# Optimization experiments

Hardware: AMD Instinct MI355X
Metric: run time of the kernel (lower is better)

## Reference

```python
import jax, jax.numpy as jnp
import numpy as np

UNITS = 1024
IN_DIM = 1024
BATCH = 64
SEQ = 512


def setup_inputs() -> dict:
    key = jax.random.key(0)
    k_x, k_wf, k_wb = jax.random.split(key, 3)
    x = jax.random.normal(k_x, (BATCH, SEQ, IN_DIM), dtype=jnp.float32)
    # keras 'random_normal' initializer -> stddev 0.05
    W_fwd = jax.random.normal(k_wf, (IN_DIM + UNITS, 4 * UNITS), dtype=jnp.float32) * 0.05
    b_fwd = jnp.zeros((4 * UNITS,), dtype=jnp.float32)
    W_bwd = jax.random.normal(k_wb, (IN_DIM + UNITS, 4 * UNITS), dtype=jnp.float32) * 0.05
    b_bwd = jnp.zeros((4 * UNITS,), dtype=jnp.float32)
    return {"x": x, "W_fwd": W_fwd, "b_fwd": b_fwd, "W_bwd": W_bwd, "b_bwd": b_bwd}


def _lstm_scan(x_tbd, W, b, units, reverse):
    # x_tbd: [T, B, D] time-major
    B = x_tbd.shape[1]
    h0 = jnp.zeros((B, units), dtype=x_tbd.dtype)
    c0 = jnp.zeros((B, units), dtype=x_tbd.dtype)

    def step(carry, x_t):
        h, c = carry
        z = jnp.concatenate([x_t, h], axis=-1) @ W + b  # [B, 4U]
        zi, zf, zo, zg = jnp.split(z, 4, axis=-1)
        c_new = jax.nn.sigmoid(zf) * c + jax.nn.sigmoid(zi) * jnp.tanh(zg)
        h_new = jax.nn.sigmoid(zo) * jnp.tanh(c_new)
        return (h_new, c_new), h_new

    _, hs = jax.lax.scan(step, (h0, c0), x_tbd, reverse=reverse)
    return hs  # [T, B, U], aligned with input time order


def reference(x, W_fwd, b_fwd, W_bwd, b_bwd):
    x_tbd = jnp.transpose(x, (1, 0, 2))  # [T, B, D]
    h_fwd = _lstm_scan(x_tbd, W_fwd, b_fwd, UNITS, reverse=False)
    h_bwd = _lstm_scan(x_tbd, W_bwd, b_bwd, UNITS, reverse=True)
    h = jnp.concatenate([h_fwd, h_bwd], axis=-1)  # [T, B, 2U]
    return jnp.transpose(h, (1, 0, 2))  # [B, T, 2U]
```

## Files before the change

kernel.cpp:

```cpp
#include <hip/hip_runtime.h>
#include <stdint.h>

#define B_ 64
#define T_ 512
#define D_ 1024
#define U_ 1024
#define G4_ 4096
#define M_ (B_ * T_)
#define ZLD 65

typedef unsigned short u16;
typedef float f32x4 __attribute__((ext_vector_type(4)));
typedef _Float16 f16x8 __attribute__((ext_vector_type(8)));
typedef unsigned short u16x4 __attribute__((ext_vector_type(4)));

__device__ __forceinline__ u16 f2h(float f) {
  union { _Float16 h; u16 u; } v; v.h = (_Float16)f; return v.u;
}
__device__ __forceinline__ float h2f(uint32_t u) {
  union { _Float16 h; u16 u; } v; v.u = (u16)u; return (float)v.h;
}
__device__ __forceinline__ float sigm(float x) { return 1.f / (1.f + __expf(-x)); }
__device__ __forceinline__ float tanhf_(float x) {
  x = fminf(12.f, fmaxf(-12.f, x));
  float e = __expf(2.f * x);
  return (e - 1.f) / (e + 1.f);
}

__device__ __forceinline__ void glds16(const void* g, void* l) {
  __builtin_amdgcn_global_load_lds(
      (const __attribute__((address_space(1))) uint32_t*)g,
      (__attribute__((address_space(3))) uint32_t*)l, 16, 0, 0);
}

template <int R>
__device__ __forceinline__ void stage_tile(const char* gbase, long gs, char* lds, int tid) {
  const int lane = tid & 63, wid = tid >> 6;
#pragma unroll
  for (int j = wid; j < R / 8; j += 4) {
    const int row = j * 8 + (lane >> 3);
    const int lg = ((lane & 7) * 16) ^ ((row & 7) << 4);
    glds16(gbase + (long)row * gs + lg, lds + j * 1024);
  }
}

__device__ __forceinline__ f16x8 read_frag(const char* lds, int row, int kbyte) {
  const int ph = row * 128 + (kbyte ^ ((row & 7) << 4));
  return *(const f16x8*)(lds + ph);
}

#define MFMA_(a, b, c) __builtin_amdgcn_mfma_f32_16x16x32_f16(a, b, c, 0, 0, 0)


__global__ __launch_bounds__(256) void cast_x_kernel(const float* __restrict__ x,
                                                     u16* __restrict__ xb) {
  const long n = (long)M_ * D_ / 4;
  for (long i = (long)blockIdx.x * blockDim.x + threadIdx.x; i < n;
       i += (long)gridDim.x * blockDim.x) {
    f32x4 v = ((const f32x4*)x)[i];
    u16x4 r;
#pragma unroll
    for (int j = 0; j < 4; ++j) r[j] = f2h(v[j]);
    ((u16x4*)xb)[i] = r;
  }
}

__global__ __launch_bounds__(256) void pack_wx_kernel(const float* __restrict__ Wf,
                                                      const float* __restrict__ Wb,
                                                      u16* __restrict__ wxT) {
  const int idx = blockIdx.x * 256 + threadIdx.x;
  const int p = idx & 4095;
  const int kc = (idx >> 12) & 63;
  const int d = (idx >> 18) & 1;
  const float* W = d ? Wb : Wf;
  const int orig = ((p >> 4) & 3) * 1024 + ((p >> 6) << 4) + (p & 15);
  u16* dst = wxT + ((long)d * G4_ + p) * 1024 + kc * 16;
  const float* src = W + (long)(kc * 16) * G4_ + orig;
#pragma unroll
  for (int j = 0; j < 16; ++j) dst[j] = f2h(src[(long)j * G4_]);
}

__global__ __launch_bounds__(256) void pack_whfl_kernel(const float* __restrict__ Wf,
                                                        const float* __restrict__ Wb,
                                                        u16* __restrict__ whfl) {
  const int idx = blockIdx.x * 256 + threadIdx.x;
  const int l = idx & 63;
  const int f = (idx >> 6) & 15;
  const int cc = (idx >> 10) & 7;
  const int ub = (idx >> 13) & 63;
  const int d = (idx >> 19) & 1;
  const float* W = d ? Wb : Wf;
  const int ni = f >> 2, kkl = f & 3;
  const int ocol = ni * 1024 + ub * 16 + (l & 15);
  const int krow = 1024 + cc * 128 + kkl * 32 + (l >> 4) * 8;
  u16* dst = whfl + ((((long)(d * 64 + ub) * 8 + cc) * 16 + f) << 9) + l * 8;
  const float* src = W + (long)krow * G4_ + ocol;
#pragma unroll
  for (int j = 0; j < 8; ++j) dst[j] = f2h(src[(long)j * G4_]);
}

__global__ __launch_bounds__(256) void gemm_xproj2(const u16* __restrict__ xbf,
                                                   const u16* __restrict__ wT,
                                                   const float* __restrict__ bF,
                                                   const float* __restrict__ bB,
                                                   u16* __restrict__ xp2) {
  __shared__ __align__(16) char smem[64 * 1024];
  const int tid = threadIdx.x, lane = tid & 63, wid = tid >> 6;
  const int wr = wid >> 1, wc = wid & 1;
  const int tm = blockIdx.x * 128, tn = blockIdx.y * 128, d = blockIdx.z;
  const char* Ag = (const char*)xbf + (long)tm * 2048;
  const char* Bg = (const char*)wT + ((long)d * G4_ + tn) * 2048;

  f32x4 acc[4][4];
#pragma unroll
  for (int mi = 0; mi < 4; ++mi)
#pragma unroll
    for (int ni = 0; ni < 4; ++ni)
#pragma unroll
      for (int v = 0; v < 4; ++v) acc[mi][ni][v] = 0.f;

  stage_tile<128>(Ag, 2048, smem, tid);
  stage_tile<128>(Bg, 2048, smem + 32768, tid);
  __syncthreads();
  const int rA = lane & 15, kb = (lane >> 4) * 16;

  for (int cc = 0; cc < 16; ++cc) {
    const int cur = cc & 1;
    char* Ac = smem + cur * 16384;
    char* Bc = smem + 32768 + cur * 16384;
    if (cc + 1 < 16) {
      stage_tile<128>(Ag + (cc + 1) * 128, 2048, smem + (cur ^ 1) * 16384, tid);
      stage_tile<128>(Bg + (cc + 1) * 128, 2048, smem + 32768 + (cur ^ 1) * 16384, tid);
    }
    f16x8 aF[4][2], bFr[4][2];
#pragma unroll
    for (int mi = 0; mi < 4; ++mi)
#pragma unroll
      for (int ks = 0; ks < 2; ++ks)
        aF[mi][ks] = read_frag(Ac, wr * 64 + mi * 16 + rA, kb + ks * 64);
#pragma unroll
    for (int ni = 0; ni < 4; ++ni)
#pragma unroll
      for (int ks = 0; ks < 2; ++ks)
        bFr[ni][ks] = read_frag(Bc, wc * 64 + ni * 16 + rA, kb + ks * 64);
#pragma unroll
    for (int mi = 0; mi < 4; ++mi)
#pragma unroll
      for (int ni = 0; ni < 4; ++ni)
#pragma unroll
        for (int ks = 0; ks < 2; ++ks)
          acc[mi][ni] = MFMA_(aF[mi][ks], bFr[ni][ks], acc[mi][ni]);
    __syncthreads();
  }

  const float* bias = d ? bB : bF;
#pragma unroll
  for (int ni = 0; ni < 4; ++ni) {
    const int p = tn + wc * 64 + ni * 16 + rA;
    const int orig = ((p >> 4) & 3) * 1024 + ((p >> 6) << 4) + (p & 15);
    const float bv = bias[orig];
    const int ub2 = p >> 6, pl = p & 63;
#pragma unroll
    for (int mi = 0; mi < 4; ++mi) {
      const int m0 = tm + wr * 64 + mi * 16 + (lane >> 4) * 4;
#pragma unroll
      for (int v = 0; v < 4; ++v) {
        const int m = m0 + v, b = m >> 9, t = m & 511;
        const int bh = b >> 5, br = b & 31;
        xp2[(((((long)d * T_ + t) * 64 + ub2) * 2 + bh) * 32 + br) * 64 + pl] =
            f2h(acc[mi][ni][v] + bv);
      }
    }
  }
}


__device__ __forceinline__ void stage_hA(const char* g, char* lds, int tid) {
  const int lane = tid & 63, wid = tid >> 6;
#pragma unroll
  for (int q = 0; q < 16; ++q) {
    const int idx = wid + q * 4;
    const int row = idx * 8 + (lane >> 3);
    const int off = ((lane & 7) * 16) ^ (((row >> 4) & 7) << 4);
    glds16(g + (long)row * 128 + off, lds + idx * 1024);
  }
}

__device__ __forceinline__ void stage_Bc(const char* wfl, int cc, char* slot, int tid) {
  const int lane = tid & 63, wid = tid >> 6;
#pragma unroll
  for (int q = 0; q < 4; ++q) {
    const int f = wid * 4 + q;
    glds16(wfl + (long)cc * 16384 + f * 1024 + lane * 16, slot + f * 1024);
  }
}

template <int CC>
__device__ __forceinline__ void kstep(char* smem, const char* wfl, int tid,
                                      int wr, int wc, int rA, int kq,
                                      f32x4 (&acc)[2]) {
  constexpr int REM = 7 - CC;
  constexpr int N = 4 * (REM < 3 ? REM : 3);
  asm volatile("s_waitcnt vmcnt(%0)" :: "i"(N) : "memory");
  __builtin_amdgcn_s_barrier();
  asm volatile("" ::: "memory");
  const char* A = smem;
  const char* Bslot = smem + 65536 + (CC & 3) * 16384;
  const int lane16 = (tid & 63) << 4;
  f16x8 aF[4], bF[2][4];
  const int br = wr * 16 + rA;
#pragma unroll
  for (int ks = 0; ks < 4; ++ks) {
    const int kbyte = CC * 256 + ks * 64 + kq * 16;
    aF[ks] = *(const f16x8*)(A + br * 2048 + (kbyte ^ ((br & 7) << 4)));
  }
#pragma unroll
  for (int ni = 0; ni < 2; ++ni)
#pragma unroll
    for (int ks = 0; ks < 4; ++ks)
      bF[ni][ks] = *(const f16x8*)(Bslot + ((wc * 2 + ni) * 4 + ks) * 1024 + lane16);
#pragma unroll
  for (int ni = 0; ni < 2; ++ni)
#pragma unroll
    for (int ks = 0; ks < 4; ++ks)
      acc[ni] = MFMA_(aF[ks], bF[ni][ks], acc[ni]);
  asm volatile("s_waitcnt lgkmcnt(0)" ::: "memory");
  __builtin_amdgcn_sched_barrier(0);
  __builtin_amdgcn_s_barrier();
  asm volatile("" ::: "memory");
  if (CC + 4 < 8)
    stage_Bc(wfl, CC + 4, smem + 65536 + ((CC + 4) & 3) * 16384, tid);
}

__global__ __launch_bounds__(256) void lstm_step8(
    const u16* __restrict__ whfl, const u16* __restrict__ xp2,
    const u16* __restrict__ h_read, u16* __restrict__ h_write,
    float* __restrict__ cst, float* __restrict__ out, int s) {
  __shared__ __align__(16) char smem[131072 + ZLD * 32 * 4];
  float* zbuf = (float*)(smem + 131072);
  const int tid = threadIdx.x, lane = tid & 63, wid = tid >> 6;
  const int wr = wid >> 1, wc = wid & 1;
  const int g = blockIdx.x, ub = g >> 1, d = g & 1, bh = blockIdx.y;
  const int t = d ? (T_ - 1 - s) : s;
  const char* hA = (const char*)h_read + ((long)d * B_ + bh * 32) * 2048;
  const char* wfl = (const char*)whfl + ((long)(d * 64 + ub) << 17);
  const char* xg = (const char*)xp2 + ((((long)d * T_ + t) * 64 + ub) * 2 + bh) * 4096;
  const int rA = lane & 15, kq = lane >> 4;

  const int bl_g = tid >> 3, ui_g = (tid & 7) * 2;
  const int u_g = ub * 16 + ui_g;
  const int bglob = bh * 32 + bl_g;

  uint32_t xr[4];
  const char* xt = xg + (bl_g * 64 + ui_g) * 2;
#define XL(gg)                                                          \
  asm volatile("global_load_dword %0, %1, off offset:%2"               \
               : "=v"(xr[gg]) : "v"(xt), "n"(gg * 32) : "memory")
  XL(0); XL(1); XL(2); XL(3);
#undef XL
  stage_hA(hA, smem, tid);
#pragma unroll
  for (int c0 = 0; c0 < 4; ++c0)
    stage_Bc(wfl, c0, smem + 65536 + c0 * 16384, tid);

  const float2 creg = *(const float2*)(cst + ((long)d * B_ + bglob) * 1024 + u_g);

  f32x4 acc[2];
#pragma unroll
  for (int ni = 0; ni < 2; ++ni)
#pragma unroll
    for (int v = 0; v < 4; ++v) acc[ni][v] = 0.f;

  kstep<0>(smem, wfl, tid, wr, wc, rA, kq, acc);
  kstep<1>(smem, wfl, tid, wr, wc, rA, kq, acc);
  kstep<2>(smem, wfl, tid, wr, wc, rA, kq, acc);
  kstep<3>(smem, wfl, tid, wr, wc, rA, kq, acc);
  kstep<4>(smem, wfl, tid, wr, wc, rA, kq, acc);
  kstep<5>(smem, wfl, tid, wr, wc, rA, kq, acc);
  kstep<6>(smem, wfl, tid, wr, wc, rA, kq, acc);
  kstep<7>(smem, wfl, tid, wr, wc, rA, kq, acc);

#pragma unroll
  for (int ni = 0; ni < 2; ++ni)
#pragma unroll
    for (int v = 0; v < 4; ++v) {
      const int row = wr * 16 + kq * 4 + v;
      const int col = (wc * 2 + ni) * 16 + rA;
      zbuf[row * ZLD + col] = acc[ni][v];
    }
  __syncthreads();

  {
    const float* zb = zbuf + bl_g * ZLD + ui_g;
    const float zi0 = zb[0]  + h2f(xr[0] & 0xffff);
    const float zi1 = zb[1]  + h2f(xr[0] >> 16);
    const float zf0 = zb[16] + h2f(xr[1] & 0xffff);
    const float zf1 = zb[17] + h2f(xr[1] >> 16);
    const float zo0 = zb[32] + h2f(xr[2] & 0xffff);
    const float zo1 = zb[33] + h2f(xr[2] >> 16);
    const float zg0 = zb[48] + h2f(xr[3] & 0xffff);
    const float zg1 = zb[49] + h2f(xr[3] >> 16);
    const float cn0 = sigm(zf0) * creg.x + sigm(zi0) * tanhf_(zg0);
    const float cn1 = sigm(zf1) * creg.y + sigm(zi1) * tanhf_(zg1);
    const float hn0 = sigm(zo0) * tanhf_(cn0);
    const float hn1 = sigm(zo1) * tanhf_(cn1);

    float2 cw; cw.x = cn0; cw.y = cn1;
    *(float2*)(cst + ((long)d * B_ + bglob) * 1024 + u_g) = cw;
    const uint32_t hv = (uint32_t)f2h(hn0) | ((uint32_t)f2h(hn1) << 16);
    *(uint32_t*)(h_write + ((long)d * B_ + bglob) * 1024 + u_g) = hv;
    float2 o2; o2.x = hn0; o2.y = hn1;
    *(float2*)(out + ((long)bglob * T_ + t) * 2048 + d * 1024 + u_g) = o2;
  }
}


extern "C" void kernel_launch(void* const* d_in, const int* in_sizes, int n_in,
                              void* d_out, int out_size, void* d_ws, size_t ws_size,
                              hipStream_t stream) {
  const float* x = (const float*)d_in[0];
  const float* Wf = (const float*)d_in[1];
  const float* bfp = (const float*)d_in[2];
  const float* Wb = (const float*)d_in[3];
  const float* bbp = (const float*)d_in[4];
  float* out = (float*)d_out;
  char* ws = (char*)d_ws;

  size_t off = 0;
  auto alloc = [&](size_t bytes) {
    char* p = ws + off;
    off = (off + bytes + 255) & ~(size_t)255;
    return p;
  };
  u16* xbf = (u16*)alloc((size_t)M_ * D_ * 2);
  u16* wxT = (u16*)alloc((size_t)2 * G4_ * 1024 * 2);
  u16* whfl = (u16*)alloc((size_t)2 * 64 * 128 * 1024);
  u16* hst = (u16*)alloc((size_t)2 * 2 * B_ * U_ * 2);
  float* cst = (float*)alloc((size_t)2 * B_ * U_ * 4);
  u16* xproj = (u16*)alloc((size_t)2 * B_ * T_ * G4_ * 2);

  hipMemsetAsync(hst, 0, (size_t)2 * 2 * B_ * U_ * 2, stream);
  hipMemsetAsync(cst, 0, (size_t)2 * B_ * U_ * 4, stream);

  cast_x_kernel<<<2048, 256, 0, stream>>>(x, xbf);
  pack_wx_kernel<<<2048, 256, 0, stream>>>(Wf, Wb, wxT);
  pack_whfl_kernel<<<4096, 256, 0, stream>>>(Wf, Wb, whfl);

  dim3 gg(M_ / 128, G4_ / 128, 2);
  gemm_xproj2<<<gg, 256, 0, stream>>>(xbf, wxT, bfp, bbp, xproj);

  for (int s = 0; s < T_; ++s) {
    const u16* hr = hst + (size_t)(s & 1) * 2 * B_ * U_;
    u16* hw = hst + (size_t)((s + 1) & 1) * 2 * B_ * U_;
    lstm_step8<<<dim3(128, 2), 256, 0, stream>>>(whfl, xproj, hr, hw, cst, out, s);
  }
}
```

Before: 3.999 ms.

## Load h fragments directly to registers and split K across warps

The per-timestep recurrent kernel stops staging h through LDS. Each lane loads its A fragments straight from global memory into registers, and all of the W_h tile is staged into LDS in one pass instead of a 4-slot ring. The work is re-split so pairs of warps each take half of K, with the partial sums reduced through the LDS z buffer. This removes the eight barrier-separated k-steps and their pipelined waits, which is where the serial per-step latency was spent. The cost is one long wait for all loads before any MFMA starts, plus higher register use for 16 fragment vectors.

```diff
diff --git a/kernel.cpp b/kernel.cpp
--- a/kernel.cpp
+++ b/kernel.cpp
@@ -50,6 +50,7 @@
 }
 
 #define MFMA_(a, b, c) __builtin_amdgcn_mfma_f32_16x16x32_f16(a, b, c, 0, 0, 0)
+#define BAR_LGKM() asm volatile("s_waitcnt lgkmcnt(0)\n\ts_barrier" ::: "memory")
 
 
 __global__ __launch_bounds__(256) void cast_x_kernel(const float* __restrict__ x,
@@ -174,78 +175,19 @@
   }
 }
 
-
-__device__ __forceinline__ void stage_hA(const char* g, char* lds, int tid) {
-  const int lane = tid & 63, wid = tid >> 6;
-#pragma unroll
-  for (int q = 0; q < 16; ++q) {
-    const int idx = wid + q * 4;
-    const int row = idx * 8 + (lane >> 3);
-    const int off = ((lane & 7) * 16) ^ (((row >> 4) & 7) << 4);
-    glds16(g + (long)row * 128 + off, lds + idx * 1024);
-  }
-}
-
-__device__ __forceinline__ void stage_Bc(const char* wfl, int cc, char* slot, int tid) {
-  const int lane = tid & 63, wid = tid >> 6;
-#pragma unroll
-  for (int q = 0; q < 4; ++q) {
-    const int f = wid * 4 + q;
-    glds16(wfl + (long)cc * 16384 + f * 1024 + lane * 16, slot + f * 1024);
-  }
-}
-
-template <int CC>
-__device__ __forceinline__ void kstep(char* smem, const char* wfl, int tid,
-                                      int wr, int wc, int rA, int kq,
-                                      f32x4 (&acc)[2]) {
-  constexpr int REM = 7 - CC;
-  constexpr int N = 4 * (REM < 3 ? REM : 3);
-  asm volatile("s_waitcnt vmcnt(%0)" :: "i"(N) : "memory");
-  __builtin_amdgcn_s_barrier();
-  asm volatile("" ::: "memory");
-  const char* A = smem;
-  const char* Bslot = smem + 65536 + (CC & 3) * 16384;
-  const int lane16 = (tid & 63) << 4;
-  f16x8 aF[4], bF[2][4];
-  const int br = wr * 16 + rA;
-#pragma unroll
-  for (int ks = 0; ks < 4; ++ks) {
-    const int kbyte = CC * 256 + ks * 64 + kq * 16;
-    aF[ks] = *(const f16x8*)(A + br * 2048 + (kbyte ^ ((br & 7) << 4)));
-  }
-#pragma unroll
-  for (int ni = 0; ni < 2; ++ni)
-#pragma unroll
-    for (int ks = 0; ks < 4; ++ks)
-      bF[ni][ks] = *(const f16x8*)(Bslot + ((wc * 2 + ni) * 4 + ks) * 1024 + lane16);
-#pragma unroll
-  for (int ni = 0; ni < 2; ++ni)
-#pragma unroll
-    for (int ks = 0; ks < 4; ++ks)
-      acc[ni] = MFMA_(aF[ks], bF[ni][ks], acc[ni]);
-  asm volatile("s_waitcnt lgkmcnt(0)" ::: "memory");
-  __builtin_amdgcn_sched_barrier(0);
-  __builtin_amdgcn_s_barrier();
-  asm volatile("" ::: "memory");
-  if (CC + 4 < 8)
-    stage_Bc(wfl, CC + 4, smem + 65536 + ((CC + 4) & 3) * 16384, tid);
-}
-
-__global__ __launch_bounds__(256) void lstm_step8(
+__global__ __launch_bounds__(256) void lstm_step9(
     const u16* __restrict__ whfl, const u16* __restrict__ xp2,
     const u16* __restrict__ h_read, u16* __restrict__ h_write,
     float* __restrict__ cst, float* __restrict__ out, int s) {
   __shared__ __align__(16) char smem[131072 + ZLD * 32 * 4];
   float* zbuf = (float*)(smem + 131072);
   const int tid = threadIdx.x, lane = tid & 63, wid = tid >> 6;
-  const int wr = wid >> 1, wc = wid & 1;
+  const int wm = wid & 1, kh = wid >> 1;
   const int g = blockIdx.x, ub = g >> 1, d = g & 1, bh = blockIdx.y;
   const int t = d ? (T_ - 1 - s) : s;
-  const char* hA = (const char*)h_read + ((long)d * B_ + bh * 32) * 2048;
+  const int rA = lane & 15, kq = lane >> 4;
   const char* wfl = (const char*)whfl + ((long)(d * 64 + ub) << 17);
   const char* xg = (const char*)xp2 + ((((long)d * T_ + t) * 64 + ub) * 2 + bh) * 4096;
-  const int rA = lane & 15, kq = lane >> 4;
 
   const int bl_g = tid >> 3, ui_g = (tid & 7) * 2;
   const int u_g = ub * 16 + ui_g;
@@ -258,37 +200,62 @@
                : "=v"(xr[gg]) : "v"(xt), "n"(gg * 32) : "memory")
   XL(0); XL(1); XL(2); XL(3);
 #undef XL
-  stage_hA(hA, smem, tid);
-#pragma unroll
-  for (int c0 = 0; c0 < 4; ++c0)
-    stage_Bc(wfl, c0, smem + 65536 + c0 * 16384, tid);
-
+  const char* ah_base =
+      (const char*)h_read +
+      (((long)d * B_ + bh * 32 + wm * 16 + rA) * 1024 + kh * 512 + kq * 8) * 2;
+  f16x8 ah[16];
+#define AH(i)                                                           \
+  asm volatile("global_load_dwordx4 %0, %1, off offset:%2"             \
+               : "=v"(ah[i]) : "v"(ah_base), "n"(i * 64) : "memory")
+  AH(0); AH(1); AH(2); AH(3); AH(4); AH(5); AH(6); AH(7);
+  AH(8); AH(9); AH(10); AH(11); AH(12); AH(13); AH(14); AH(15);
+#undef AH
+#pragma unroll
+  for (int q = 0; q < 32; ++q) {
+    const int f = wid * 32 + q;
+    glds16(wfl + (long)f * 1024 + lane * 16, smem + f * 1024);
+  }
   const float2 creg = *(const float2*)(cst + ((long)d * B_ + bglob) * 1024 + u_g);
 
-  f32x4 acc[2];
-#pragma unroll
-  for (int ni = 0; ni < 2; ++ni)
+  asm volatile("s_waitcnt vmcnt(0)" ::: "memory");
+  __builtin_amdgcn_sched_barrier(0);
+  __builtin_amdgcn_s_barrier();
+  asm volatile("" ::: "memory");
+
+  f32x4 acc[4];
+#pragma unroll
+  for (int ni = 0; ni < 4; ++ni)
 #pragma unroll
     for (int v = 0; v < 4; ++v) acc[ni][v] = 0.f;
-
-  kstep<0>(smem, wfl, tid, wr, wc, rA, kq, acc);
-  kstep<1>(smem, wfl, tid, wr, wc, rA, kq, acc);
-  kstep<2>(smem, wfl, tid, wr, wc, rA, kq, acc);
-  kstep<3>(smem, wfl, tid, wr, wc, rA, kq, acc);
-  kstep<4>(smem, wfl, tid, wr, wc, rA, kq, acc);
-  kstep<5>(smem, wfl, tid, wr, wc, rA, kq, acc);
-  kstep<6>(smem, wfl, tid, wr, wc, rA, kq, acc);
-  kstep<7>(smem, wfl, tid, wr, wc, rA, kq, acc);
-
-#pragma unroll
-  for (int ni = 0; ni < 2; ++ni)
-#pragma unroll
-    for (int v = 0; v < 4; ++v) {
-      const int row = wr * 16 + kq * 4 + v;
-      const int col = (wc * 2 + ni) * 16 + rA;
-      zbuf[row * ZLD + col] = acc[ni][v];
+  const char* bb = smem + (kh << 16) + (lane << 4);
+#pragma unroll
+  for (int kk = 0; kk < 16; ++kk) {
+#pragma unroll
+    for (int ni = 0; ni < 4; ++ni) {
+      const f16x8 bF =
+          *(const f16x8*)(bb + (((kk >> 2) * 16 + ni * 4 + (kk & 3)) << 10));
+      acc[ni] = MFMA_(ah[kk], bF, acc[ni]);
     }
-  __syncthreads();
+  }
+
+  if (kh == 1) {
+#pragma unroll
+    for (int ni = 0; ni < 4; ++ni)
+#pragma unroll
+      for (int v = 0; v < 4; ++v)
+        zbuf[(wm * 16 + kq * 4 + v) * ZLD + ni * 16 + rA] = acc[ni][v];
+  }
+  BAR_LGKM();
+  if (kh == 0) {
+#pragma unroll
+    for (int ni = 0; ni < 4; ++ni)
+#pragma unroll
+      for (int v = 0; v < 4; ++v) {
+        const int ix = (wm * 16 + kq * 4 + v) * ZLD + ni * 16 + rA;
+        zbuf[ix] += acc[ni][v];
+      }
+  }
+  BAR_LGKM();
 
   {
     const float* zb = zbuf + bl_g * ZLD + ui_g;
@@ -352,6 +319,6 @@
   for (int s = 0; s < T_; ++s) {
     const u16* hr = hst + (size_t)(s & 1) * 2 * B_ * U_;
     u16* hw = hst + (size_t)((s + 1) & 1) * 2 * B_ * U_;
-    lstm_step8<<<dim3(128, 2), 256, 0, stream>>>(whfl, xproj, hr, hw, cst, out, s);
-  }
-}
+    lstm_step9<<<dim3(128, 2), 256, 0, stream>>>(whfl, xproj, hr, hw, cst, out, s);
+  }
+}
```

Result: slower. 4.871 ms (+21.8%).

## Split recurrent step into 16-row batch tiles with smaller LDS footprint

Applied to the files above, without the earlier changes.

The per-timestep LSTM kernel now tiles the batch into four 16-row slices instead of two 32-row slices, doubling the grid to 512 blocks. Each wave computes one 16x16 gate tile. The weight staging buffer shrinks from four slots to a double buffer, so two blocks can fit per CU, and the xproj layout is changed to match the finer batch split. The aim is better CU occupancy and latency hiding in a launch-bound, latency-dominated recurrent step. In exchange, every block re-reads the same recurrent weight slice from global memory twice as often, and the shallower prefetch exposes more load latency.

```diff
diff --git a/kernel.cpp b/kernel.cpp
--- a/kernel.cpp
+++ b/kernel.cpp
@@ -166,8 +166,7 @@
 #pragma unroll
       for (int v = 0; v < 4; ++v) {
         const int m = m0 + v, b = m >> 9, t = m & 511;
-        const int bh = b >> 5, br = b & 31;
-        xp2[(((((long)d * T_ + t) * 64 + ub2) * 2 + bh) * 32 + br) * 64 + pl] =
+        xp2[((((long)d * T_ + t) * 64 + ub2) * 64 + b) * 64 + pl] =
             f2h(acc[mi][ni][v] + bv);
       }
     }
@@ -175,11 +174,11 @@
 }
 
 
-__device__ __forceinline__ void stage_hA(const char* g, char* lds, int tid) {
+__device__ __forceinline__ void stage_hA16(const char* g, char* lds, int tid) {
   const int lane = tid & 63, wid = tid >> 6;
 #pragma unroll
-  for (int q = 0; q < 16; ++q) {
-    const int idx = wid + q * 4;
+  for (int q = 0; q < 8; ++q) {
+    const int idx = wid * 8 + q;
     const int row = idx * 8 + (lane >> 3);
     const int off = ((lane & 7) * 16) ^ (((row >> 4) & 7) << 4);
     glds16(g + (long)row * 128 + off, lds + idx * 1024);
@@ -196,121 +195,100 @@
 }
 
 template <int CC>
-__device__ __forceinline__ void kstep(char* smem, const char* wfl, int tid,
-                                      int wr, int wc, int rA, int kq,
-                                      f32x4 (&acc)[2]) {
-  constexpr int REM = 7 - CC;
-  constexpr int N = 4 * (REM < 3 ? REM : 3);
+__device__ __forceinline__ void kstepv(char* smem, const char* wfl, int tid,
+                                       int wg, int rA, int kq, f32x4& acc) {
+  constexpr int N = (CC < 7) ? 4 : 0;
   asm volatile("s_waitcnt vmcnt(%0)" :: "i"(N) : "memory");
   __builtin_amdgcn_s_barrier();
   asm volatile("" ::: "memory");
   const char* A = smem;
-  const char* Bslot = smem + 65536 + (CC & 3) * 16384;
+  const char* Bslot = smem + 32768 + (CC & 1) * 16384;
   const int lane16 = (tid & 63) << 4;
-  f16x8 aF[4], bF[2][4];
-  const int br = wr * 16 + rA;
+  f16x8 aF[4], bF[4];
 #pragma unroll
   for (int ks = 0; ks < 4; ++ks) {
     const int kbyte = CC * 256 + ks * 64 + kq * 16;
-    aF[ks] = *(const f16x8*)(A + br * 2048 + (kbyte ^ ((br & 7) << 4)));
-  }
-#pragma unroll
-  for (int ni = 0; ni < 2; ++ni)
-#pragma unroll
-    for (int ks = 0; ks < 4; ++ks)
-      bF[ni][ks] = *(const f16x8*)(Bslot + ((wc * 2 + ni) * 4 + ks) * 1024 + lane16);
-#pragma unroll
-  for (int ni = 0; ni < 2; ++ni)
-#pragma unroll
-    for (int ks = 0; ks < 4; ++ks)
-      acc[ni] = MFMA_(aF[ks], bF[ni][ks], acc[ni]);
+    aF[ks] = *(const f16x8*)(A + rA * 2048 + (kbyte ^ ((rA & 7) << 4)));
+  }
+#pragma unroll
+  for (int ks = 0; ks < 4; ++ks)
+    bF[ks] = *(const f16x8*)(Bslot + (wg * 4 + ks) * 1024 + lane16);
+#pragma unroll
+  for (int ks = 0; ks < 4; ++ks)
+    acc = MFMA_(aF[ks], bF[ks], acc);
   asm volatile("s_waitcnt lgkmcnt(0)" ::: "memory");
   __builtin_amdgcn_sched_barrier(0);
   __builtin_amdgcn_s_barrier();
   asm volatile("" ::: "memory");
-  if (CC + 4 < 8)
-    stage_Bc(wfl, CC + 4, smem + 65536 + ((CC + 4) & 3) * 16384, tid);
-}
-
-__global__ __launch_bounds__(256) void lstm_step8(
+  if (CC + 2 < 8)
+    stage_Bc(wfl, CC + 2, smem + 32768 + (CC & 1) * 16384, tid);
+}
+
+__global__ __launch_bounds__(256, 2) void lstm_step12(
     const u16* __restrict__ whfl, const u16* __restrict__ xp2,
     const u16* __restrict__ h_read, u16* __restrict__ h_write,
     float* __restrict__ cst, float* __restrict__ out, int s) {
-  __shared__ __align__(16) char smem[131072 + ZLD * 32 * 4];
-  float* zbuf = (float*)(smem + 131072);
-  const int tid = threadIdx.x, lane = tid & 63, wid = tid >> 6;
-  const int wr = wid >> 1, wc = wid & 1;
+  __shared__ __align__(16) char smem[32768 + 32768 + ZLD * 16 * 4];
+  float* zbuf = (float*)(smem + 65536);
+  const int tid = threadIdx.x, lane = tid & 63, wg = tid >> 6;
   const int g = blockIdx.x, ub = g >> 1, d = g & 1, bh = blockIdx.y;
   const int t = d ? (T_ - 1 - s) : s;
-  const char* hA = (const char*)h_read + ((long)d * B_ + bh * 32) * 2048;
+  const int rA = lane & 15, kq = lane >> 4;
   const char* wfl = (const char*)whfl + ((long)(d * 64 + ub) << 17);
-  const char* xg = (const char*)xp2 + ((((long)d * T_ + t) * 64 + ub) * 2 + bh) * 4096;
-  const int rA = lane & 15, kq = lane >> 4;
-
-  const int bl_g = tid >> 3, ui_g = (tid & 7) * 2;
+  const char* hA = (const char*)h_read + ((long)d * B_ + bh * 16) * 2048;
+
+  const int row_g = tid >> 4, ui_g = tid & 15;
+  const int bglob = bh * 16 + row_g;
   const int u_g = ub * 16 + ui_g;
-  const int bglob = bh * 32 + bl_g;
-
+
+  float creg;
+  {
+    const float* cp = cst + ((long)d * B_ + bglob) * 1024 + u_g;
+    asm volatile("global_load_dword %0, %1, off" : "=v"(creg) : "v"(cp) : "memory");
+  }
   uint32_t xr[4];
-  const char* xt = xg + (bl_g * 64 + ui_g) * 2;
-#define XL(gg)                                                          \
-  asm volatile("global_load_dword %0, %1, off offset:%2"               \
+  {
+    const char* xt = (const char*)xp2 +
+        (((((long)d * T_ + t) * 64 + ub) * 64 + bglob) * 64 + ui_g) * 2;
+#define XL(gg)                                                            \
+  asm volatile("global_load_ushort %0, %1, off offset:%2"                 \
                : "=v"(xr[gg]) : "v"(xt), "n"(gg * 32) : "memory")
-  XL(0); XL(1); XL(2); XL(3);
+    XL(0); XL(1); XL(2); XL(3);
 #undef XL
-  stage_hA(hA, smem, tid);
-#pragma unroll
-  for (int c0 = 0; c0 < 4; ++c0)
-    stage_Bc(wfl, c0, smem + 65536 + c0 * 16384, tid);
-
-  const float2 creg = *(const float2*)(cst + ((long)d * B_ + bglob) * 1024 + u_g);
-
-  f32x4 acc[2];
-#pragma unroll
-  for (int ni = 0; ni < 2; ++ni)
-#pragma unroll
-    for (int v = 0; v < 4; ++v) acc[ni][v] = 0.f;
-
-  kstep<0>(smem, wfl, tid, wr, wc, rA, kq, acc);
-  kstep<1>(smem, wfl, tid, wr, wc, rA, kq, acc);
-  kstep<2>(smem, wfl, tid, wr, wc, rA, kq, acc);
-  kstep<3>(smem, wfl, tid, wr, wc, rA, kq, acc);
-  kstep<4>(smem, wfl, tid, wr, wc, rA, kq, acc);
-  kstep<5>(smem, wfl, tid, wr, wc, rA, kq, acc);
-  kstep<6>(smem, wfl, tid, wr, wc, rA, kq, acc);
-  kstep<7>(smem, wfl, tid, wr, wc, rA, kq, acc);
-
-#pragma unroll
-  for (int ni = 0; ni < 2; ++ni)
-#pragma unroll
-    for (int v = 0; v < 4; ++v) {
-      const int row = wr * 16 + kq * 4 + v;
-      const int col = (wc * 2 + ni) * 16 + rA;
-      zbuf[row * ZLD + col] = acc[ni][v];
-    }
+  }
+  stage_hA16(hA, smem, tid);
+  stage_Bc(wfl, 0, smem + 32768, tid);
+  stage_Bc(wfl, 1, smem + 32768 + 16384, tid);
+
+  f32x4 acc;
+#pragma unroll
+  for (int v = 0; v < 4; ++v) acc[v] = 0.f;
+
+  kstepv<0>(smem, wfl, tid, wg, rA, kq, acc);
+  kstepv<1>(smem, wfl, tid, wg, rA, kq, acc);
+  kstepv<2>(smem, wfl, tid, wg, rA, kq, acc);
+  kstepv<3>(smem, wfl, tid, wg, rA, kq, acc);
+  kstepv<4>(smem, wfl, tid, wg, rA, kq, acc);
+  kstepv<5>(smem, wfl, tid, wg, rA, kq, acc);
+  kstepv<6>(smem, wfl, tid, wg, rA, kq, acc);
+  kstepv<7>(smem, wfl, tid, wg, rA, kq, acc);
+
+#pragma unroll
+  for (int v = 0; v < 4; ++v)
+    zbuf[(kq * 4 + v) * ZLD + wg * 16 + rA] = acc[v];
   __syncthreads();
 
   {
-    const float* zb = zbuf + bl_g * ZLD + ui_g;
-    const float zi0 = zb[0]  + h2f(xr[0] & 0xffff);
-    const float zi1 = zb[1]  + h2f(xr[0] >> 16);
-    const float zf0 = zb[16] + h2f(xr[1] & 0xffff);
-    const float zf1 = zb[17] + h2f(xr[1] >> 16);
-    const float zo0 = zb[32] + h2f(xr[2] & 0xffff);
-    const float zo1 = zb[33] + h2f(xr[2] >> 16);
-    const float zg0 = zb[48] + h2f(xr[3] & 0xffff);
-    const float zg1 = zb[49] + h2f(xr[3] >> 16);
-    const float cn0 = sigm(zf0) * creg.x + sigm(zi0) * tanhf_(zg0);
-    const float cn1 = sigm(zf1) * creg.y + sigm(zi1) * tanhf_(zg1);
-    const float hn0 = sigm(zo0) * tanhf_(cn0);
-    const float hn1 = sigm(zo1) * tanhf_(cn1);
-
-    float2 cw; cw.x = cn0; cw.y = cn1;
-    *(float2*)(cst + ((long)d * B_ + bglob) * 1024 + u_g) = cw;
-    const uint32_t hv = (uint32_t)f2h(hn0) | ((uint32_t)f2h(hn1) << 16);
-    *(uint32_t*)(h_write + ((long)d * B_ + bglob) * 1024 + u_g) = hv;
-    float2 o2; o2.x = hn0; o2.y = hn1;
-    *(float2*)(out + ((long)bglob * T_ + t) * 2048 + d * 1024 + u_g) = o2;
+    const float* zb = zbuf + row_g * ZLD + ui_g;
+    const float zi = zb[0]  + h2f(xr[0]);
+    const float zf = zb[16] + h2f(xr[1]);
+    const float zo = zb[32] + h2f(xr[2]);
+    const float zg = zb[48] + h2f(xr[3]);
+    const float cn = sigm(zf) * creg + sigm(zi) * tanhf_(zg);
+    const float hn = sigm(zo) * tanhf_(cn);
+    cst[((long)d * B_ + bglob) * 1024 + u_g] = cn;
+    h_write[((long)d * B_ + bglob) * 1024 + u_g] = f2h(hn);
+    out[((long)bglob * T_ + t) * 2048 + d * 1024 + u_g] = hn;
   }
 }
 
@@ -352,6 +330,6 @@
   for (int s = 0; s < T_; ++s) {
     const u16* hr = hst + (size_t)(s & 1) * 2 * B_ * U_;
     u16* hw = hst + (size_t)((s + 1) & 1) * 2 * B_ * U_;
-    lstm_step8<<<dim3(128, 2), 256, 0, stream>>>(whfl, xproj, hr, hw, cst, out, s);
-  }
-}
+    lstm_step12<<<dim3(128, 4), 256, 0, stream>>>(whfl, xproj, hr, hw, cst, out, s);
+  }
+}
```

Measured after the change: 4.165 ms. 1.04x slower.
